# Kernel tuning notes

Measured on AMD Instinct MI355X. Metric: run time of the kernel, lower is better.

Reference implementation:

```python
import jax, jax.numpy as jnp
import numpy as np

B, T, H, S, E, TGT = 8192, 24, 256, 256, 256, 1
IN = 2  # temporal value + mask concatenated


def setup_inputs() -> dict:
    key = jax.random.key(0)
    ks = jax.random.split(key, 20)
    f = jnp.float32
    sc = 0.05
    return {
        "static_feature": jax.random.normal(ks[0], (B, S), f),
        "temporal_feature": jax.random.normal(ks[1], (B, T), f),
        "temporal_mask": (jax.random.uniform(ks[2], (B, T)) < 0.5).astype(f),
        "targets": (jax.random.uniform(ks[3], (B, TGT)) < 0.5).astype(f),
        # fixed random initial hidden/cell state (created in __init__)
        "h0": jax.random.normal(ks[4], (B, H), f),
        "c0": jax.random.normal(ks[5], (B, H), f),
        # LSTMCell params (torch gate order: i, f, g, o)
        "W_ih": jax.random.normal(ks[6], (4 * H, IN), f) * sc,
        "W_hh": jax.random.normal(ks[7], (4 * H, H), f) * sc,
        "b_ih": jax.random.normal(ks[8], (4 * H,), f) * sc,
        "b_hh": jax.random.normal(ks[9], (4 * H,), f) * sc,
        # static-branch MLP
        "W1": jax.random.normal(ks[10], (E, S), f) * sc,
        "b1": jnp.zeros((E,), f),
        "W2": jax.random.normal(ks[11], (E, E), f) * sc,
        "b2": jnp.zeros((E,), f),
        "W3": jax.random.normal(ks[12], (E, E), f) * sc,
        "b3": jnp.zeros((E,), f),
        # final classifier over concat(h, s)
        "W_lr": jax.random.normal(ks[13], (TGT, E + H), f) * sc,
        "b_lr": jnp.zeros((TGT,), f),
    }


def _lstm_step(W_ih, W_hh, b_ih, b_hh):
    def step(carry, xt):
        h, c = carry
        gates = xt @ W_ih.T + b_ih + h @ W_hh.T + b_hh  # [B, 4H]
        i, fg, g, o = jnp.split(gates, 4, axis=-1)
        i = jax.nn.sigmoid(i)
        fg = jax.nn.sigmoid(fg)
        g = jnp.tanh(g)
        o = jax.nn.sigmoid(o)
        c = fg * c + i * g
        h = o * jnp.tanh(c)
        return (h, c), None
    return step


def reference(static_feature, temporal_feature, temporal_mask, targets,
              h0, c0, W_ih, W_hh, b_ih, b_hh,
              W1, b1, W2, b2, W3, b3, W_lr, b_lr):
    # [B, T, 2] -> scan over time: [T, B, 2]
    xs = jnp.swapaxes(jnp.stack([temporal_feature, temporal_mask], axis=-1), 0, 1)
    (h, c), _ = jax.lax.scan(_lstm_step(W_ih, W_hh, b_ih, b_hh), (h0, c0), xs)

    # static MLP (dropout in eval mode = identity)
    s = jax.nn.relu(static_feature @ W1.T + b1)
    s = jax.nn.relu(s @ W2.T + b2)
    s = jax.nn.relu(s @ W3.T + b3)

    predicts = jnp.concatenate([h, s], axis=1) @ W_lr.T + b_lr  # [B, TGT]
    # numerically stable BCEWithLogits, mean reduction
    loss = jnp.mean(jnp.maximum(predicts, 0) - predicts * targets
                    + jnp.log1p(jnp.exp(-jnp.abs(predicts))))
    return predicts, loss
```

## Files before the change

kernel.cpp:

```cpp
#include <hip/hip_runtime.h>

typedef _Float16 f16;
typedef _Float16 f16x8 __attribute__((ext_vector_type(8)));
typedef float f32x16 __attribute__((ext_vector_type(16)));

#define MFMA32(A, B, C) __builtin_amdgcn_mfma_f32_32x32x16_f16((A), (B), (C), 0, 0, 0)

__device__ __forceinline__ float sigm_(float x) {
    return __builtin_amdgcn_rcpf(1.f + __builtin_amdgcn_exp2f(-1.44269504088896f * x));
}
__device__ __forceinline__ float tanh_(float x) {
    float e = __builtin_amdgcn_exp2f(2.88539008177793f * x);
    return 1.f - 2.f * __builtin_amdgcn_rcpf(1.f + e);
}

__device__ __forceinline__ void stage16(const void* g, void* s) {
    __builtin_amdgcn_global_load_lds(
        (const __attribute__((address_space(1))) unsigned int*)(g),
        (__attribute__((address_space(3))) unsigned int*)(s), 16, 0, 0);
}

__device__ __forceinline__ int afi(int kt, int lp) {
    return (kt << 6) + (lp ^ (((lp >> 3) ^ kt) & 7));
}

__global__ void frag_conv_all(const float* __restrict__ Whh,
                              const float* __restrict__ W1,
                              const float* __restrict__ W2,
                              const float* __restrict__ W3,
                              f16* __restrict__ dst) {
    int idx = blockIdx.x * blockDim.x + threadIdx.x;
    if (idx < 262144) {
        int e  = idx & 7;
        int lp = (idx >> 3) & 63;
        int nt = (idx >> 9) & 31;
        int kt = idx >> 14;
        int j = (nt << 5) + (lp & 31);
        int k = (kt << 4) + ((lp >> 5) << 3) + e;
        dst[idx] = (f16)Whh[j * 256 + k];
    } else {
        int r   = idx - 262144;
        int sel = r >> 16;
        int i   = r & 65535;
        const float* W = (sel == 0) ? W1 : (sel == 1) ? W2 : W3;
        int e  = i & 7;
        int lp = (i >> 3) & 63;
        int kt = (i >> 9) & 15;
        int nt = i >> 13;
        int j = (nt << 5) + (lp & 31);
        int k = (kt << 4) + ((lp >> 5) << 3) + e;
        dst[idx] = (f16)W[j * 256 + k];
    }
}

#define STAGE4(PN, SRCOFF) do {                                              \
        const char* _g = sb + (SRCOFF);                                      \
        stage16(_g,         (PN) + st_o        );                            \
        stage16(_g +  8192, (PN) + st_o +  4096);                            \
        stage16(_g + 16384, (PN) + st_o +  8192);                            \
        stage16(_g + 24576, (PN) + st_o + 12288);                            \
    } while (0)

#define PHASE(KT, PC, PN) do {                                               \
        STAGE4(PN, (((KT) + 2) & 15) * 32768);                               \
        asm volatile("s_waitcnt vmcnt(8)" ::: "memory");                     \
        __builtin_amdgcn_sched_barrier(0);                                   \
        f16x8 Av  = *(const f16x8*)(Acur + afi(KT, l) * 8);                  \
        f16x8 Bv0 = *(const f16x8*)((PC) + ((0 * 8 + w) << 9) + (l << 3));   \
        f16x8 Bv1 = *(const f16x8*)((PC) + ((1 * 8 + w) << 9) + (l << 3));   \
        f16x8 Bv2 = *(const f16x8*)((PC) + ((2 * 8 + w) << 9) + (l << 3));   \
        f16x8 Bv3 = *(const f16x8*)((PC) + ((3 * 8 + w) << 9) + (l << 3));   \
        acc0 = MFMA32(Av, Bv0, acc0);                                        \
        acc1 = MFMA32(Av, Bv1, acc1);                                        \
        acc2 = MFMA32(Av, Bv2, acc2);                                        \
        acc3 = MFMA32(Av, Bv3, acc3);                                        \
    } while (0)

__global__ __launch_bounds__(512)
void lstm_fused(const float* __restrict__ statf,
                const float* __restrict__ tfg,
                const float* __restrict__ tmg,
                const float* __restrict__ h0,
                const float* __restrict__ c0,
                const float* __restrict__ Wih,
                const float* __restrict__ bih,
                const float* __restrict__ bhh,
                const float* __restrict__ b1,
                const float* __restrict__ b2,
                const float* __restrict__ b3,
                const float* __restrict__ Wlr,
                const float* __restrict__ blr,
                const f16* __restrict__ WBH,
                const f16* __restrict__ WB1,
                const f16* __restrict__ WB2,
                const f16* __restrict__ WB3,
                float* __restrict__ out)
{
    __shared__ __align__(16) f16 wsl[3][16384];
    __shared__ __align__(16) f16 Afb[2][1024][8];
    __shared__ float tf_l[32][24];
    __shared__ float tm_l[32][24];
    __shared__ float wlr_l[512];
    __shared__ f16   xa_l[1024];
    __shared__ f16   xb_l[1024];
    __shared__ float xc_l[1024];

    const int tid = threadIdx.x;
    const int w   = tid >> 6;
    const int l   = tid & 63;
    const int b0  = blockIdx.x * 32;

    const char* sb  = (const char*)WBH + (w << 10) + (l << 4);
    const int   st_o = (w << 9) + (l << 3);

    {
        f16* s0 = &wsl[0][0];
        f16* s1 = &wsl[1][0];
        #pragma unroll
        for (int i = 0; i < 4; ++i) stage16(sb + i * 8192,         s0 + st_o + i * 4096);
        #pragma unroll
        for (int i = 0; i < 4; ++i) stage16(sb + 32768 + i * 8192, s1 + st_o + i * 4096);
    }

    for (int i = tid; i < 32 * 24; i += 512) {
        int r = i / 24, t = i - r * 24;
        tf_l[r][t] = tfg[(b0 + r) * 24 + t];
        tm_l[r][t] = tmg[(b0 + r) * 24 + t];
    }
    wlr_l[tid] = Wlr[tid];
    for (int i = tid; i < 1024; i += 512) {
        xa_l[i] = (f16)Wih[2 * i];
        xb_l[i] = (f16)Wih[2 * i + 1];
        xc_l[i] = bih[i] + bhh[i];
    }
    for (int i = tid; i < 1024; i += 512) {
        int fr = i >> 6, lp = i & 63;
        int row  = lp & 31;
        int koff = (fr << 4) + ((lp >> 5) << 3);
        const float4* s4 = (const float4*)&h0[(b0 + row) * 256 + koff];
        float4 a = s4[0], b = s4[1];
        f16x8 v;
        v[0]=(f16)a.x; v[1]=(f16)a.y; v[2]=(f16)a.z; v[3]=(f16)a.w;
        v[4]=(f16)b.x; v[5]=(f16)b.y; v[6]=(f16)b.z; v[7]=(f16)b.w;
        *(f16x8*)(&Afb[0][afi(fr, lp)][0]) = v;
    }

    const int jc = (w << 5) + (l & 31);
    float cst[16];
    #pragma unroll
    for (int reg = 0; reg < 16; ++reg) {
        int bl = (reg & 3) + ((reg >> 2) << 3) + ((l >> 5) << 2);
        cst[reg] = c0[(b0 + bl) * 256 + jc];
    }
    const int wkt    = jc >> 4;
    const int wlp_hi = ((l >> 3) & 1) << 5;
    const int we     = l & 7;

    asm volatile("s_waitcnt lgkmcnt(0)" ::: "memory");
    __builtin_amdgcn_s_barrier();

    f16* p0 = &wsl[0][0];
    f16* p1 = &wsl[1][0];
    f16* p2 = &wsl[2][0];

    #pragma unroll 1
    for (int t = 0; t < 24; ++t) {
        f16* Acur = &Afb[t & 1][0][0];
        f16* Anxt = &Afb[(t + 1) & 1][0][0];
        f32x16 acc0, acc1, acc2, acc3;
        {
            const float xcv0 = xc_l[jc],       xcv1 = xc_l[256 + jc];
            const float xcv2 = xc_l[512 + jc], xcv3 = xc_l[768 + jc];
            #pragma unroll
            for (int e = 0; e < 16; ++e) {
                acc0[e] = xcv0; acc1[e] = xcv1; acc2[e] = xcv2; acc3[e] = xcv3;
            }
        }

        PHASE(0,  p0, p2);  PHASE(1,  p1, p0);  PHASE(2,  p2, p1);
        PHASE(3,  p0, p2);  PHASE(4,  p1, p0);  PHASE(5,  p2, p1);
        PHASE(6,  p0, p2);  PHASE(7,  p1, p0);  PHASE(8,  p2, p1);
        PHASE(9,  p0, p2);  PHASE(10, p1, p0);  PHASE(11, p2, p1);
        PHASE(12, p0, p2);  PHASE(13, p1, p0);  PHASE(14, p2, p1);
        PHASE(15, p0, p2);

        __builtin_amdgcn_sched_barrier(0);

        {
            const float xav0 = (float)xa_l[jc],       xav1 = (float)xa_l[256 + jc];
            const float xav2 = (float)xa_l[512 + jc], xav3 = (float)xa_l[768 + jc];
            const float xbv0 = (float)xb_l[jc],       xbv1 = (float)xb_l[256 + jc];
            const float xbv2 = (float)xb_l[512 + jc], xbv3 = (float)xb_l[768 + jc];
            #pragma unroll
            for (int reg = 0; reg < 16; ++reg) {
                const int   bl  = (reg & 3) + ((reg >> 2) << 3) + ((l >> 5) << 2);
                const float tfv = tf_l[bl][t];
                const float tmv = tm_l[bl][t];
                float gi = acc0[reg] + xav0 * tfv + xbv0 * tmv;
                float gf = acc1[reg] + xav1 * tfv + xbv1 * tmv;
                float gg = acc2[reg] + xav2 * tfv + xbv2 * tmv;
                float go = acc3[reg] + xav3 * tfv + xbv3 * tmv;
                float i_ = sigm_(gi);
                float f_ = sigm_(gf);
                float g_ = tanh_(gg);
                float o_ = sigm_(go);
                float c_ = f_ * cst[reg] + i_ * g_;
                cst[reg] = c_;
                float h_ = o_ * tanh_(c_);
                Anxt[afi(wkt, bl | wlp_hi) * 8 + we] = (f16)h_;
            }
        }
        asm volatile("s_waitcnt lgkmcnt(0)" ::: "memory");
        __builtin_amdgcn_s_barrier();
        __builtin_amdgcn_sched_barrier(0);

        f16* tp = p0; p0 = p1; p1 = p2; p2 = tp;
    }

    asm volatile("s_waitcnt vmcnt(0)" ::: "memory");
    __builtin_amdgcn_s_barrier();

    f16* A2 = &wsl[0][0];
    f16* A3 = &wsl[0][8192];

    for (int i = tid; i < 1024; i += 512) {
        int fr = i >> 6, lp = i & 63;
        int row  = lp & 31;
        int koff = (fr << 4) + ((lp >> 5) << 3);
        const float4* s4 = (const float4*)&statf[(b0 + row) * 256 + koff];
        float4 a = s4[0], b = s4[1];
        f16x8 v;
        v[0]=(f16)a.x; v[1]=(f16)a.y; v[2]=(f16)a.z; v[3]=(f16)a.w;
        v[4]=(f16)b.x; v[5]=(f16)b.y; v[6]=(f16)b.z; v[7]=(f16)b.w;
        *(f16x8*)(A2 + afi(fr, lp) * 8) = v;
    }
    __syncthreads();

    {
        const f16*   WBl[3]  = {WB1, WB2, WB3};
        const float* bls[3]  = {b1, b2, b3};
        f16*         ains[3] = {A2, A3, A2};
        f16*         aous[3] = {A3, A2, A3};
        const int lane8 = l << 3;
        #pragma unroll 1
        for (int layer = 0; layer < 3; ++layer) {
            const f16* WL  = WBl[layer];
            f16* ain  = ains[layer];
            f16* aout = aous[layer];
            float bias = bls[layer][jc];
            f32x16 acc2;
            #pragma unroll
            for (int e = 0; e < 16; ++e) acc2[e] = bias;

            f16x8 Bq[2], Aq2[2];
            Bq[0]  = *(const f16x8*)(WL + ((w * 16 + 0) * 512) + lane8);
            Aq2[0] = *(const f16x8*)(ain + afi(0, l) * 8);
            #pragma unroll
            for (int kt = 0; kt < 16; ++kt) {
                const int cb = kt & 1, nb = cb ^ 1;
                if (kt < 15) {
                    Bq[nb]  = *(const f16x8*)(WL + ((w * 16 + (kt + 1)) * 512) + lane8);
                    Aq2[nb] = *(const f16x8*)(ain + afi(kt + 1, l) * 8);
                }
                acc2 = MFMA32(Aq2[cb], Bq[cb], acc2);
            }
            __syncthreads();
            #pragma unroll
            for (int reg = 0; reg < 16; ++reg) {
                float v = acc2[reg];
                v = v > 0.f ? v : 0.f;
                const int bl2 = (reg & 3) + ((reg >> 2) << 3) + ((l >> 5) << 2);
                aout[afi(wkt, bl2 | wlp_hi) * 8 + we] = (f16)v;
            }
            __syncthreads();
        }
    }

    {
        const int r  = (w << 2) + (l >> 4);
        const int lg = l & 15;
        const int lp = r | (((lg >> 3) & 1) << 5);
        const int ee = lg & 7;
        float sum = 0.f;
        #pragma unroll
        for (int i = 0; i < 16; ++i) {
            int j = lg + (i << 4);
            float hv = (float)Afb[0][afi(i, lp)][ee];
            float sv = (float)A3[afi(i, lp) * 8 + ee];
            sum += hv * wlr_l[j] + sv * wlr_l[256 + j];
        }
        sum += __shfl_xor(sum, 8);
        sum += __shfl_xor(sum, 4);
        sum += __shfl_xor(sum, 2);
        sum += __shfl_xor(sum, 1);
        if (lg == 0) out[b0 + r] = sum + blr[0];
    }
}

__global__ __launch_bounds__(1024)
void bce_kernel(const float* __restrict__ pred, const float* __restrict__ tgt,
                float* __restrict__ lossp) {
    const int tid = threadIdx.x;
    float acc = 0.f;
    for (int i = tid; i < 8192; i += 1024) {
        float p  = pred[i];
        float t  = tgt[i];
        float ax = fabsf(p);
        acc += fmaxf(p, 0.f) - p * t
             + log1pf(__builtin_amdgcn_exp2f(-1.44269504088896f * ax));
    }
    #pragma unroll
    for (int m = 32; m >= 1; m >>= 1) acc += __shfl_xor(acc, m);
    __shared__ float red[16];
    if ((tid & 63) == 0) red[tid >> 6] = acc;
    __syncthreads();
    if (tid < 16) {
        float v = red[tid];
        #pragma unroll
        for (int m = 8; m >= 1; m >>= 1) v += __shfl_xor(v, m);
        if (tid == 0) lossp[0] = v * (1.f / 8192.f);
    }
}

extern "C" void kernel_launch(void* const* d_in, const int* in_sizes, int n_in,
                              void* d_out, int out_size, void* d_ws, size_t ws_size,
                              hipStream_t stream) {
    const float* statf = (const float*)d_in[0];
    const float* tfg   = (const float*)d_in[1];
    const float* tmg   = (const float*)d_in[2];
    const float* tgt   = (const float*)d_in[3];
    const float* h0    = (const float*)d_in[4];
    const float* c0    = (const float*)d_in[5];
    const float* Wih   = (const float*)d_in[6];
    const float* Whh   = (const float*)d_in[7];
    const float* bih   = (const float*)d_in[8];
    const float* bhh   = (const float*)d_in[9];
    const float* W1    = (const float*)d_in[10];
    const float* b1    = (const float*)d_in[11];
    const float* W2    = (const float*)d_in[12];
    const float* b2    = (const float*)d_in[13];
    const float* W3    = (const float*)d_in[14];
    const float* b3    = (const float*)d_in[15];
    const float* Wlr   = (const float*)d_in[16];
    const float* blr   = (const float*)d_in[17];
    float* out = (float*)d_out;

    f16* WBH = (f16*)d_ws;
    f16* WB1 = WBH + 262144;
    f16* WB2 = WB1 + 65536;
    f16* WB3 = WB2 + 65536;

    frag_conv_all<<<896, 512, 0, stream>>>(Whh, W1, W2, W3, WBH);

    lstm_fused<<<256, 512, 0, stream>>>(statf, tfg, tmg, h0, c0, Wih, bih, bhh,
                                        b1, b2, b3, Wlr, blr,
                                        WBH, WB1, WB2, WB3, out);

    bce_kernel<<<1, 1024, 0, stream>>>(out, tgt, out + 8192);
}
```

Measured before the change: 315.6 us.

## Load LSTM recurrent weights directly into registers instead of staging through LDS

Replaces the triple-buffered global→LDS async staging of W_hh fragments with direct global loads into registers, double-buffered two k-steps ahead and issued right after each MFMA group. This removes the LDS round-trip and its vmcnt waits for the B operand. It relies on L2/L1 caching, since every block re-reads the whole recurrent weight matrix from global memory each timestep. A padding shared array and waves_per_eu(2,2) are added to pin occupancy at two blocks per CU, and the MLP scratch moves into its own buffer.

```diff
diff --git a/kernel.cpp b/kernel.cpp
--- a/kernel.cpp
+++ b/kernel.cpp
@@ -12,12 +12,6 @@
 __device__ __forceinline__ float tanh_(float x) {
     float e = __builtin_amdgcn_exp2f(2.88539008177793f * x);
     return 1.f - 2.f * __builtin_amdgcn_rcpf(1.f + e);
-}
-
-__device__ __forceinline__ void stage16(const void* g, void* s) {
-    __builtin_amdgcn_global_load_lds(
-        (const __attribute__((address_space(1))) unsigned int*)(g),
-        (__attribute__((address_space(3))) unsigned int*)(s), 16, 0, 0);
 }
 
 __device__ __forceinline__ int afi(int kt, int lp) {
@@ -53,73 +47,75 @@
     }
 }
 
-#define STAGE4(PN, SRCOFF) do {                                              \
-        const char* _g = sb + (SRCOFF);                                      \
-        stage16(_g,         (PN) + st_o        );                            \
-        stage16(_g +  8192, (PN) + st_o +  4096);                            \
-        stage16(_g + 16384, (PN) + st_o +  8192);                            \
-        stage16(_g + 24576, (PN) + st_o + 12288);                            \
+#define PHASE(KT, B0, B1, B2, B3) do {                                       \
+        f16x8 Av = *(const f16x8*)(Acur + afi((KT), l) * 8);                 \
+        acc0 = MFMA32(Av, B0, acc0);                                         \
+        acc1 = MFMA32(Av, B1, acc1);                                         \
+        acc2 = MFMA32(Av, B2, acc2);                                         \
+        acc3 = MFMA32(Av, B3, acc3);                                         \
+        {                                                                    \
+            const f16* _wp = wb + ((((KT) + 2) & 15) * 16384);               \
+            B0 = *(const f16x8*)(_wp);                                       \
+            B1 = *(const f16x8*)(_wp + 4096);                                \
+            B2 = *(const f16x8*)(_wp + 8192);                                \
+            B3 = *(const f16x8*)(_wp + 12288);                               \
+        }                                                                    \
+        __builtin_amdgcn_sched_barrier(0);                                   \
     } while (0)
 
-#define PHASE(KT, PC, PN) do {                                               \
-        STAGE4(PN, (((KT) + 2) & 15) * 32768);                               \
-        asm volatile("s_waitcnt vmcnt(8)" ::: "memory");                     \
-        __builtin_amdgcn_sched_barrier(0);                                   \
-        f16x8 Av  = *(const f16x8*)(Acur + afi(KT, l) * 8);                  \
-        f16x8 Bv0 = *(const f16x8*)((PC) + ((0 * 8 + w) << 9) + (l << 3));   \
-        f16x8 Bv1 = *(const f16x8*)((PC) + ((1 * 8 + w) << 9) + (l << 3));   \
-        f16x8 Bv2 = *(const f16x8*)((PC) + ((2 * 8 + w) << 9) + (l << 3));   \
-        f16x8 Bv3 = *(const f16x8*)((PC) + ((3 * 8 + w) << 9) + (l << 3));   \
-        acc0 = MFMA32(Av, Bv0, acc0);                                        \
-        acc1 = MFMA32(Av, Bv1, acc1);                                        \
-        acc2 = MFMA32(Av, Bv2, acc2);                                        \
-        acc3 = MFMA32(Av, Bv3, acc3);                                        \
-    } while (0)
-
-__global__ __launch_bounds__(512)
-void lstm_fused(const float* __restrict__ statf,
-                const float* __restrict__ tfg,
-                const float* __restrict__ tmg,
-                const float* __restrict__ h0,
-                const float* __restrict__ c0,
-                const float* __restrict__ Wih,
-                const float* __restrict__ bih,
-                const float* __restrict__ bhh,
-                const float* __restrict__ b1,
-                const float* __restrict__ b2,
-                const float* __restrict__ b3,
-                const float* __restrict__ Wlr,
-                const float* __restrict__ blr,
-                const f16* __restrict__ WBH,
-                const f16* __restrict__ WB1,
-                const f16* __restrict__ WB2,
-                const f16* __restrict__ WB3,
-                float* __restrict__ out)
+__global__ void
+__launch_bounds__(512)
+__attribute__((amdgpu_waves_per_eu(2, 2)))
+lstm_fused(const float* __restrict__ statf,
+           const float* __restrict__ tfg,
+           const float* __restrict__ tmg,
+           const float* __restrict__ h0,
+           const float* __restrict__ c0,
+           const float* __restrict__ Wih,
+           const float* __restrict__ bih,
+           const float* __restrict__ bhh,
+           const float* __restrict__ b1,
+           const float* __restrict__ b2,
+           const float* __restrict__ b3,
+           const float* __restrict__ Wlr,
+           const float* __restrict__ blr,
+           const f16* __restrict__ WBH,
+           const f16* __restrict__ WB1,
+           const f16* __restrict__ WB2,
+           const f16* __restrict__ WB3,
+           float* __restrict__ out)
 {
-    __shared__ __align__(16) f16 wsl[3][16384];
     __shared__ __align__(16) f16 Afb[2][1024][8];
+    __shared__ __align__(16) f16 mlpA[2][8192];
     __shared__ float tf_l[32][24];
     __shared__ float tm_l[32][24];
     __shared__ float wlr_l[512];
     __shared__ f16   xa_l[1024];
     __shared__ f16   xb_l[1024];
     __shared__ float xc_l[1024];
+    __shared__ __align__(16) f16 padx[12288];
 
     const int tid = threadIdx.x;
     const int w   = tid >> 6;
     const int l   = tid & 63;
     const int b0  = blockIdx.x * 32;
 
-    const char* sb  = (const char*)WBH + (w << 10) + (l << 4);
-    const int   st_o = (w << 9) + (l << 3);
-
+    if (statf == (const float*)1) padx[0] = (f16)0.f;
+
+    const f16* wb = WBH + (w << 9) + (l << 3);
+
+    f16x8 Ba0, Ba1, Ba2, Ba3, Bb0, Bb1, Bb2, Bb3;
     {
-        f16* s0 = &wsl[0][0];
-        f16* s1 = &wsl[1][0];
-        #pragma unroll
-        for (int i = 0; i < 4; ++i) stage16(sb + i * 8192,         s0 + st_o + i * 4096);
-        #pragma unroll
-        for (int i = 0; i < 4; ++i) stage16(sb + 32768 + i * 8192, s1 + st_o + i * 4096);
+        const f16* _wp = wb;
+        Ba0 = *(const f16x8*)(_wp);
+        Ba1 = *(const f16x8*)(_wp + 4096);
+        Ba2 = *(const f16x8*)(_wp + 8192);
+        Ba3 = *(const f16x8*)(_wp + 12288);
+        _wp = wb + 16384;
+        Bb0 = *(const f16x8*)(_wp);
+        Bb1 = *(const f16x8*)(_wp + 4096);
+        Bb2 = *(const f16x8*)(_wp + 8192);
+        Bb3 = *(const f16x8*)(_wp + 12288);
     }
 
     for (int i = tid; i < 32 * 24; i += 512) {
@@ -159,10 +155,6 @@
     asm volatile("s_waitcnt lgkmcnt(0)" ::: "memory");
     __builtin_amdgcn_s_barrier();
 
-    f16* p0 = &wsl[0][0];
-    f16* p1 = &wsl[1][0];
-    f16* p2 = &wsl[2][0];
-
     #pragma unroll 1
     for (int t = 0; t < 24; ++t) {
         f16* Acur = &Afb[t & 1][0][0];
@@ -177,14 +169,14 @@
             }
         }
 
-        PHASE(0,  p0, p2);  PHASE(1,  p1, p0);  PHASE(2,  p2, p1);
-        PHASE(3,  p0, p2);  PHASE(4,  p1, p0);  PHASE(5,  p2, p1);
-        PHASE(6,  p0, p2);  PHASE(7,  p1, p0);  PHASE(8,  p2, p1);
-        PHASE(9,  p0, p2);  PHASE(10, p1, p0);  PHASE(11, p2, p1);
-        PHASE(12, p0, p2);  PHASE(13, p1, p0);  PHASE(14, p2, p1);
-        PHASE(15, p0, p2);
-
-        __builtin_amdgcn_sched_barrier(0);
+        PHASE(0,  Ba0, Ba1, Ba2, Ba3);  PHASE(1,  Bb0, Bb1, Bb2, Bb3);
+        PHASE(2,  Ba0, Ba1, Ba2, Ba3);  PHASE(3,  Bb0, Bb1, Bb2, Bb3);
+        PHASE(4,  Ba0, Ba1, Ba2, Ba3);  PHASE(5,  Bb0, Bb1, Bb2, Bb3);
+        PHASE(6,  Ba0, Ba1, Ba2, Ba3);  PHASE(7,  Bb0, Bb1, Bb2, Bb3);
+        PHASE(8,  Ba0, Ba1, Ba2, Ba3);  PHASE(9,  Bb0, Bb1, Bb2, Bb3);
+        PHASE(10, Ba0, Ba1, Ba2, Ba3);  PHASE(11, Bb0, Bb1, Bb2, Bb3);
+        PHASE(12, Ba0, Ba1, Ba2, Ba3);  PHASE(13, Bb0, Bb1, Bb2, Bb3);
+        PHASE(14, Ba0, Ba1, Ba2, Ba3);  PHASE(15, Bb0, Bb1, Bb2, Bb3);
 
         {
             const float xav0 = (float)xa_l[jc],       xav1 = (float)xa_l[256 + jc];
@@ -213,15 +205,10 @@
         asm volatile("s_waitcnt lgkmcnt(0)" ::: "memory");
         __builtin_amdgcn_s_barrier();
         __builtin_amdgcn_sched_barrier(0);
-
-        f16* tp = p0; p0 = p1; p1 = p2; p2 = tp;
-    }
-
-    asm volatile("s_waitcnt vmcnt(0)" ::: "memory");
-    __builtin_amdgcn_s_barrier();
-
-    f16* A2 = &wsl[0][0];
-    f16* A3 = &wsl[0][8192];
+    }
+
+    f16* A2 = &mlpA[0][0];
+    f16* A3 = &mlpA[1][0];
 
     for (int i = tid; i < 1024; i += 512) {
         int fr = i >> 6, lp = i & 63;
```

After: 501.9 us. +59.1%, slower.

## Split W_hh streaming between LDS staging and direct register loads, rotate k-start per block

Applied to the files above, without the earlier changes.

Each k-tile of the recurrent weight is now half staged into LDS through global_load_lds and half loaded straight into registers from global memory, double-buffered across phases. This halves the LDS weight buffers and the LDS read traffic per MFMA. Each block also starts its k-sweep at a different offset, spreading L2 accesses across blocks. The MLP activations move to a dedicated LDS buffer because the smaller weight ring can no longer hold them. Register pressure and global load latency on the direct-load path may rise in exchange.

```diff
diff --git a/kernel.cpp b/kernel.cpp
--- a/kernel.cpp
+++ b/kernel.cpp
@@ -53,27 +53,26 @@
     }
 }
 
-#define STAGE4(PN, SRCOFF) do {                                              \
-        const char* _g = sb + (SRCOFF);                                      \
-        stage16(_g,         (PN) + st_o        );                            \
-        stage16(_g +  8192, (PN) + st_o +  4096);                            \
-        stage16(_g + 16384, (PN) + st_o +  8192);                            \
-        stage16(_g + 24576, (PN) + st_o + 12288);                            \
-    } while (0)
-
-#define PHASE(KT, PC, PN) do {                                               \
-        STAGE4(PN, (((KT) + 2) & 15) * 32768);                               \
-        asm volatile("s_waitcnt vmcnt(8)" ::: "memory");                     \
-        __builtin_amdgcn_sched_barrier(0);                                   \
-        f16x8 Av  = *(const f16x8*)(Acur + afi(KT, l) * 8);                  \
-        f16x8 Bv0 = *(const f16x8*)((PC) + ((0 * 8 + w) << 9) + (l << 3));   \
-        f16x8 Bv1 = *(const f16x8*)((PC) + ((1 * 8 + w) << 9) + (l << 3));   \
-        f16x8 Bv2 = *(const f16x8*)((PC) + ((2 * 8 + w) << 9) + (l << 3));   \
-        f16x8 Bv3 = *(const f16x8*)((PC) + ((3 * 8 + w) << 9) + (l << 3));   \
-        acc0 = MFMA32(Av, Bv0, acc0);                                        \
-        acc1 = MFMA32(Av, Bv1, acc1);                                        \
-        acc2 = MFMA32(Av, Bv2, acc2);                                        \
-        acc3 = MFMA32(Av, Bv3, acc3);                                        \
+#define PHASE(KT, PC, PN, B0, B1) do {                                        \
+        const int _s2 = ((KT) + 2 + rot) & 15;                                \
+        const char* _g = sbL + _s2 * 32768;                                   \
+        stage16(_g,        (PN) + dL0);                                       \
+        stage16(_g + 8192, (PN) + dL0 + 4096);                                \
+        asm volatile("s_waitcnt vmcnt(6)" ::: "memory");                      \
+        __builtin_amdgcn_sched_barrier(0);                                    \
+        f16x8 Av = *(const f16x8*)(Acur + afi(((KT) + rot) & 15, l) * 8);     \
+        f16x8 L0 = *(const f16x8*)((PC) + dL0);                               \
+        f16x8 L1 = *(const f16x8*)((PC) + dL0 + 4096);                        \
+        acc0 = MFMA32(Av, L0, acc0);                                          \
+        acc1 = MFMA32(Av, L1, acc1);                                          \
+        acc2 = MFMA32(Av, B0, acc2);                                          \
+        acc3 = MFMA32(Av, B1, acc3);                                          \
+        {                                                                     \
+            const f16* _r = WBH + _s2 * 16384 + rOff;                         \
+            B0 = *(const f16x8*)(_r);                                         \
+            B1 = *(const f16x8*)(_r + 4096);                                  \
+        }                                                                     \
+        __builtin_amdgcn_sched_barrier(0);                                    \
     } while (0)
 
 __global__ __launch_bounds__(512)
@@ -96,8 +95,9 @@
                 const f16* __restrict__ WB3,
                 float* __restrict__ out)
 {
-    __shared__ __align__(16) f16 wsl[3][16384];
+    __shared__ __align__(16) f16 wsl[3][8192];
     __shared__ __align__(16) f16 Afb[2][1024][8];
+    __shared__ __align__(16) f16 mlpA[2][8192];
     __shared__ float tf_l[32][24];
     __shared__ float tm_l[32][24];
     __shared__ float wlr_l[512];
@@ -109,18 +109,11 @@
     const int w   = tid >> 6;
     const int l   = tid & 63;
     const int b0  = blockIdx.x * 32;
-
-    const char* sb  = (const char*)WBH + (w << 10) + (l << 4);
-    const int   st_o = (w << 9) + (l << 3);
-
-    {
-        f16* s0 = &wsl[0][0];
-        f16* s1 = &wsl[1][0];
-        #pragma unroll
-        for (int i = 0; i < 4; ++i) stage16(sb + i * 8192,         s0 + st_o + i * 4096);
-        #pragma unroll
-        for (int i = 0; i < 4; ++i) stage16(sb + 32768 + i * 8192, s1 + st_o + i * 4096);
-    }
+    const int rot = blockIdx.x & 15;
+
+    const char* sbL = (const char*)WBH + (w << 10) + (l << 4);
+    const int dL0 = (w << 9) + (l << 3);
+    const int rOff = 8192 + (w << 9) + (l << 3);
 
     for (int i = tid; i < 32 * 24; i += 512) {
         int r = i / 24, t = i - r * 24;
@@ -156,12 +149,31 @@
     const int wlp_hi = ((l >> 3) & 1) << 5;
     const int we     = l & 7;
 
-    asm volatile("s_waitcnt lgkmcnt(0)" ::: "memory");
+    asm volatile("s_waitcnt vmcnt(0) lgkmcnt(0)" ::: "memory");
     __builtin_amdgcn_s_barrier();
 
     f16* p0 = &wsl[0][0];
     f16* p1 = &wsl[1][0];
     f16* p2 = &wsl[2][0];
+
+    f16x8 Bc0, Bc1, Bd0, Bd1;
+    {
+        const int s0 = rot, s1 = (rot + 1) & 15;
+        stage16(sbL + s0 * 32768,        p0 + dL0);
+        stage16(sbL + s0 * 32768 + 8192, p0 + dL0 + 4096);
+        __builtin_amdgcn_sched_barrier(0);
+        const f16* r0 = WBH + s0 * 16384 + rOff;
+        Bc0 = *(const f16x8*)(r0);
+        Bc1 = *(const f16x8*)(r0 + 4096);
+        __builtin_amdgcn_sched_barrier(0);
+        stage16(sbL + s1 * 32768,        p1 + dL0);
+        stage16(sbL + s1 * 32768 + 8192, p1 + dL0 + 4096);
+        __builtin_amdgcn_sched_barrier(0);
+        const f16* r1 = WBH + s1 * 16384 + rOff;
+        Bd0 = *(const f16x8*)(r1);
+        Bd1 = *(const f16x8*)(r1 + 4096);
+        __builtin_amdgcn_sched_barrier(0);
+    }
 
     #pragma unroll 1
     for (int t = 0; t < 24; ++t) {
@@ -177,12 +189,14 @@
             }
         }
 
-        PHASE(0,  p0, p2);  PHASE(1,  p1, p0);  PHASE(2,  p2, p1);
-        PHASE(3,  p0, p2);  PHASE(4,  p1, p0);  PHASE(5,  p2, p1);
-        PHASE(6,  p0, p2);  PHASE(7,  p1, p0);  PHASE(8,  p2, p1);
-        PHASE(9,  p0, p2);  PHASE(10, p1, p0);  PHASE(11, p2, p1);
-        PHASE(12, p0, p2);  PHASE(13, p1, p0);  PHASE(14, p2, p1);
-        PHASE(15, p0, p2);
+        PHASE(0,  p0, p2, Bc0, Bc1);  PHASE(1,  p1, p0, Bd0, Bd1);
+        PHASE(2,  p2, p1, Bc0, Bc1);  PHASE(3,  p0, p2, Bd0, Bd1);
+        PHASE(4,  p1, p0, Bc0, Bc1);  PHASE(5,  p2, p1, Bd0, Bd1);
+        PHASE(6,  p0, p2, Bc0, Bc1);  PHASE(7,  p1, p0, Bd0, Bd1);
+        PHASE(8,  p2, p1, Bc0, Bc1);  PHASE(9,  p0, p2, Bd0, Bd1);
+        PHASE(10, p1, p0, Bc0, Bc1);  PHASE(11, p2, p1, Bd0, Bd1);
+        PHASE(12, p0, p2, Bc0, Bc1);  PHASE(13, p1, p0, Bd0, Bd1);
+        PHASE(14, p2, p1, Bc0, Bc1);  PHASE(15, p0, p2, Bd0, Bd1);
 
         __builtin_amdgcn_sched_barrier(0);
 
@@ -220,8 +234,8 @@
     asm volatile("s_waitcnt vmcnt(0)" ::: "memory");
     __builtin_amdgcn_s_barrier();
 
-    f16* A2 = &wsl[0][0];
-    f16* A3 = &wsl[0][8192];
+    f16* A2 = &mlpA[0][0];
+    f16* A3 = &mlpA[1][0];
 
     for (int i = tid; i < 1024; i += 512) {
         int fr = i >> 6, lp = i & 63;
```

Result: slower. 356.4 us (+12.9%).
